# Kernel tuning notes

Measured on AMD Instinct MI355X. Metric: run time of the kernel, lower is better.

## Reference

```python
import jax, jax.numpy as jnp
import numpy as np

B, H, W, C = 16, 112, 112, 128
WS, SS, NH = 7, 3, 4  # window_size, shift_size, num_heads
EPS = 1e-5


def _ln(x, g, b):
    m = jnp.mean(x, axis=-1, keepdims=True)
    v = jnp.var(x, axis=-1, keepdims=True)
    return (x - m) * jax.lax.rsqrt(v + EPS) * g + b


def _rel_index(w):
    # standard Swin relative-position index, [w*w, w*w] int
    coords = np.stack(np.meshgrid(np.arange(w), np.arange(w), indexing='ij'))  # [2,w,w]
    flat = coords.reshape(2, -1)                      # [2, N]
    rel = (flat[:, :, None] - flat[:, None, :]).transpose(1, 2, 0)  # [N,N,2]
    rel = rel + (w - 1)
    return rel[..., 0] * (2 * w - 1) + rel[..., 1]


def _attn_mask(Hp, Wp, w, s):
    # standard Swin shifted-window attention mask, [nW, N, N] float32 (0 / -100)
    img = np.zeros((Hp, Wp))
    cnt = 0
    for hs in (slice(0, -w), slice(-w, -s), slice(-s, None)):
        for ws_ in (slice(0, -w), slice(-w, -s), slice(-s, None)):
            img[hs, ws_] = cnt
            cnt += 1
    mw = img.reshape(Hp // w, w, Wp // w, w).transpose(0, 2, 1, 3).reshape(-1, w * w)
    d = mw[:, None, :] - mw[:, :, None]
    return np.where(d != 0, -100.0, 0.0).astype(np.float32)


def setup_inputs() -> dict:
    key = jax.random.key(0)
    ks = jax.random.split(key, 8)
    f = lambda k, shape: jax.random.normal(k, shape, dtype=jnp.float32) * 0.02
    return dict(
        x=jax.random.normal(ks[0], (B, H, W, C), dtype=jnp.float32),
        norm1_g=jnp.ones((C,), jnp.float32), norm1_b=jnp.zeros((C,), jnp.float32),
        qkv_w=f(ks[1], (C, 3 * C)), qkv_b=jnp.zeros((3 * C,), jnp.float32),
        rel_table=f(ks[2], ((2 * WS - 1) ** 2, NH)),
        proj_w=f(ks[3], (C, C)), proj_b=jnp.zeros((C,), jnp.float32),
        norm2_g=jnp.ones((C,), jnp.float32), norm2_b=jnp.zeros((C,), jnp.float32),
        fc1_w=f(ks[4], (C, 4 * C)), fc1_b=jnp.zeros((4 * C,), jnp.float32),
        fc2_w=f(ks[5], (4 * C, C)), fc2_b=jnp.zeros((C,), jnp.float32),
    )


def reference(x, norm1_g, norm1_b, qkv_w, qkv_b, rel_table, proj_w, proj_b,
              norm2_g, norm2_b, fc1_w, fc1_b, fc2_w, fc2_b):
    w, s, nH = WS, SS, NH
    hd = C // nH
    N = w * w
    scale = hd ** -0.5

    shortcut = x
    xn = _ln(x, norm1_g, norm1_b)
    # cyclic shift (H, W already multiples of w -> no padding)
    xs = jnp.roll(xn, (-s, -s), axis=(1, 2)) if s > 0 else xn
    # window partition -> [B*nW, N, C]
    wins = xs.reshape(B, H // w, w, W // w, w, C).transpose(0, 1, 3, 2, 4, 5).reshape(-1, N, C)

    qkv = wins @ qkv_w + qkv_b  # [M, N, 3C]
    q, k, v = [t.reshape(-1, N, nH, hd).transpose(0, 2, 1, 3)
               for t in jnp.split(qkv, 3, axis=-1)]
    attn = jnp.einsum('mhqd,mhkd->mhqk', q * scale, k)  # [M, nH, N, N]

    idx = _rel_index(w)  # static numpy [N, N]
    bias = rel_table[idx.reshape(-1)].reshape(N, N, nH).transpose(2, 0, 1)  # [nH, N, N]
    attn = attn + bias[None]

    if s > 0:
        mask = jnp.asarray(_attn_mask(H, W, w, s))  # [nW, N, N] static
        nW = mask.shape[0]
        attn = (attn.reshape(B, nW, nH, N, N) + mask[None, :, None]).reshape(-1, nH, N, N)

    attn = jax.nn.softmax(attn, axis=-1)
    out = jnp.einsum('mhqk,mhkd->mhqd', attn, v).transpose(0, 2, 1, 3).reshape(-1, N, C)
    out = out @ proj_w + proj_b

    # window reverse + unshift
    x_attn = out.reshape(B, H // w, W // w, w, w, C).transpose(0, 1, 3, 2, 4, 5).reshape(B, H, W, C)
    if s > 0:
        x_attn = jnp.roll(x_attn, (s, s), axis=(1, 2))

    x1 = shortcut + x_attn
    xn2 = _ln(x1, norm2_g, norm2_b)
    hdd = jax.nn.gelu(xn2 @ fc1_w + fc1_b, approximate=False)  # torch nn.GELU (exact)
    return x1 + (hdd @ fc2_w + fc2_b)
```

## Files before the change

### kernel.cpp

```cpp
#include <hip/hip_runtime.h>
#include <stdint.h>

typedef unsigned short u16;
typedef unsigned int   u32;
typedef __attribute__((ext_vector_type(8))) short bh8;
typedef __attribute__((ext_vector_type(4))) float f32x4;

#define SCALE 0.17677669529663687f
#define MFMA  __builtin_amdgcn_mfma_f32_16x16x32_bf16

#define WS_QKV  0
#define WS_PROJ 49152
#define WS_F1   65536
#define WS_F2   131072
#define WS_M    196608
#define WS_QB   327680
#define WS_S1   328448
#define WS_T1   329472

__device__ __forceinline__ u16 f2bf(float f){
    u32 i; __builtin_memcpy(&i,&f,4); i += 0x7fffu + ((i>>16)&1u); return (u16)(i>>16);
}
__device__ __forceinline__ float bflo(u32 u){
    u32 i = u << 16; float f; __builtin_memcpy(&f,&i,4); return f;
}
__device__ __forceinline__ float bfhi(u32 u){
    u32 i = u & 0xffff0000u; float f; __builtin_memcpy(&f,&i,4); return f;
}
__device__ __forceinline__ u32 cvtpk(float lo, float hi){
    u32 r; asm("v_cvt_pk_bf16_f32 %0, %1, %2" : "=v"(r) : "v"(lo), "v"(hi)); return r;
}
__device__ __forceinline__ float rcpf(float v){
    float r; asm("v_rcp_f32 %0, %1" : "=v"(r) : "v"(v)); return r;
}
__device__ __forceinline__ float gelu_f(float x){
    float ax = fabsf(x);
    float z  = ax * 0.70710678118654752f;
    float t  = rcpf(fmaf(0.3275911f, z, 1.0f));
    float p  = t * fmaf(t, fmaf(t, fmaf(t, fmaf(t, 1.061405429f, -1.453152027f),
                                        1.421413741f), -0.284496736f), 0.254829592f);
    float e  = __expf(-z * z);
    float y  = fmaf(-p, e, 1.0f);
    return fmaf(0.5f * ax, y, 0.5f * x);
}
union BH8U { bh8 v; u32 u[4]; };

__global__ void prep_k(const float* __restrict__ qkvw, const float* __restrict__ projw,
                       const float* __restrict__ f1w,  const float* __restrict__ f2w,
                       const float* __restrict__ rel,  const float* __restrict__ qkvb,
                       const float* __restrict__ n2g,  const float* __restrict__ n2b,
                       const float* __restrict__ f1b,  u16* __restrict__ ws)
{
    int idx = blockIdx.x * 256 + threadIdx.x;
    if (idx < 49152) {
        int c = idx / 384, j = idx % 384;
        float v = qkvw[idx] * (j < 128 ? SCALE : 1.0f);
        ws[WS_QKV + j * 128 + c] = f2bf(v);
    } else if (idx < 65536) {
        int i = idx - 49152; int k = i >> 7, j = i & 127;
        int pk = (k & ~31) | ((k & 15) << 1) | ((k >> 4) & 1);
        ws[WS_PROJ + j * 128 + pk] = f2bf(projw[i]);
    } else if (idx < 131072) {
        int i = idx - 65536; int c = i >> 9, j = i & 511;
        ws[WS_F1 + j * 128 + c] = f2bf(f1w[i] * n2g[c]);
    } else if (idx < 196608) {
        int i = idx - 131072; int k = i >> 7, j = i & 127;
        int pk = (k & ~31) | ((k & 15) << 1) | ((k >> 4) & 1);
        ws[WS_F2 + j * 512 + pk] = f2bf(f2w[i]);
    } else if (idx < 262144) {
        int m = idx - 196608;
        int jr = m & 3, lane = (m >> 2) & 63, tct = (m >> 8) & 15;
        int h = (m >> 12) & 3, cls = (m >> 14) & 3;
        int rt = tct >> 2, ct = tct & 3;
        int row = rt * 16 + (lane >> 4) * 4 + jr, key = ct * 16 + (lane & 15);
        float v;
        if (row < 49 && key < 49) {
            int ri = row / 7, rc = row % 7, ki = key / 7, kc = key % 7;
            v = rel[((ri - ki + 6) * 13 + (rc - kc + 6)) * 4 + h];
            int rH = (cls & 2) ? (ri < 4 ? 1 : 2) : 0, rW = (cls & 1) ? (rc < 4 ? 1 : 2) : 0;
            int kH = (cls & 2) ? (ki < 4 ? 1 : 2) : 0, kW = (cls & 1) ? (kc < 4 ? 1 : 2) : 0;
            if (rH * 3 + rW != kH * 3 + kW) v -= 100.0f;
        } else v = -30000.0f;
        ((float*)(ws + WS_M))[m] = v;
    } else if (idx < 262528) {
        int j = idx - 262144;
        ((float*)(ws + WS_QB))[j] = qkvb[j] * (j < 128 ? SCALE : 1.0f);
    } else if (idx < 263040) {
        int j = idx - 262528;
        float s1 = 0.f, t1 = 0.f;
        for (int c = 0; c < 128; ++c) {
            float w = f1w[c * 512 + j];
            s1 = fmaf(n2g[c], w, s1);
            t1 = fmaf(n2b[c], w, t1);
        }
        ((float*)(ws + WS_S1))[j] = s1;
        ((float*)(ws + WS_T1))[j] = f1b[j] + t1;
    }
}

__global__ __launch_bounds__(256, 3) void swin_attn_k(
    const float* __restrict__ x, const float* __restrict__ n1g, const float* __restrict__ n1b,
    const float* __restrict__ projb, const u16* __restrict__ ws, float* __restrict__ out)
{
    __shared__ u16 arena[16384];
    __shared__ u16 vt[9216];
    const int tid = threadIdx.x, h = tid >> 6, lane = tid & 63;
    const int c15 = lane & 15, g = lane >> 4;
    const int m = blockIdx.x, b = m >> 8, hb = (m >> 4) & 15, wb = m & 15;
    const int cls = ((hb == 15) ? 2 : 0) | ((wb == 15) ? 1 : 0);
    const float* QB = (const float*)(ws + WS_QB);
    const float* Mb = (const float*)(ws + WS_M) + (size_t)((cls * 4 + h) * 16) * 256;

    {
        const int t = h * 16 + (lane >> 2), ss = lane & 3;
        if (t < 49) {
            const int td = (t * 37) >> 8, tm = t - td * 7;
            int hs = hb * 7 + td + 3;  if (hs >= 112) hs -= 112;
            int wsw = wb * 7 + tm + 3; if (wsw >= 112) wsw -= 112;
            const float* px = x + (size_t)((b * 112 + hs) * 112 + wsw) * 128 + ss * 32;
            float4 xv[8];
            #pragma unroll
            for (int i = 0; i < 8; ++i) xv[i] = *(const float4*)(px + i * 4);
            float s = 0.f, q = 0.f;
            #pragma unroll
            for (int i = 0; i < 8; ++i) {
                s += xv[i].x + xv[i].y + xv[i].z + xv[i].w;
                q += xv[i].x*xv[i].x + xv[i].y*xv[i].y + xv[i].z*xv[i].z + xv[i].w*xv[i].w;
            }
            s += __shfl_xor(s, 1); q += __shfl_xor(q, 1);
            s += __shfl_xor(s, 2); q += __shfl_xor(q, 2);
            float mean = s * (1.f/128.f), var = q * (1.f/128.f) - mean * mean;
            float rstd = rsqrtf(var + 1e-5f);
            const float* pg = n1g + ss * 32; const float* pb = n1b + ss * 32;
            #pragma unroll
            for (int i = 0; i < 4; ++i) {
                float4 a = xv[2*i], c = xv[2*i+1];
                float4 g1 = *(const float4*)(pg + i*8),  g2 = *(const float4*)(pg + i*8 + 4);
                float4 b1 = *(const float4*)(pb + i*8),  b2 = *(const float4*)(pb + i*8 + 4);
                uint4 w;
                w.x = cvtpk((a.x-mean)*rstd*g1.x + b1.x, (a.y-mean)*rstd*g1.y + b1.y);
                w.y = cvtpk((a.z-mean)*rstd*g1.z + b1.z, (a.w-mean)*rstd*g1.w + b1.w);
                w.z = cvtpk((c.x-mean)*rstd*g2.x + b2.x, (c.y-mean)*rstd*g2.y + b2.y);
                w.w = cvtpk((c.z-mean)*rstd*g2.z + b2.z, (c.w-mean)*rstd*g2.w + b2.w);
                *(uint4*)&arena[t * 136 + ss * 32 + i * 8] = w;
            }
        } else {
            #pragma unroll
            for (int i = 0; i < 4; ++i) *(uint4*)&arena[t * 136 + (lane & 3) * 32 + i * 8] = (uint4){0,0,0,0};
        }
    }
    __syncthreads();

    {
        bh8 avf[2][4];
        #pragma unroll
        for (int jt = 0; jt < 2; ++jt)
            #pragma unroll
            for (int kc = 0; kc < 4; ++kc)
                avf[jt][kc] = *(const bh8*)&ws[WS_QKV + (256 + h*32 + jt*16 + c15)*128 + kc*32 + g*8];
        const float vb0 = QB[256 + h*32 + c15], vb1 = QB[256 + h*32 + 16 + c15];
        #pragma unroll
        for (int tt = 0; tt < 4; ++tt) {
            bh8 xf[4];
            #pragma unroll
            for (int kc = 0; kc < 4; ++kc)
                xf[kc] = *(const bh8*)&arena[(tt*16 + c15)*136 + kc*32 + g*8];
            f32x4 D0 = {0,0,0,0}, D1 = {0,0,0,0};
            #pragma unroll
            for (int kc = 0; kc < 4; ++kc) { D0 = MFMA(xf[kc], avf[0][kc], D0, 0,0,0); D1 = MFMA(xf[kc], avf[1][kc], D1, 0,0,0); }
            uint2 p0, p1;
            p0.x = cvtpk(D0[0]+vb0, D0[1]+vb0); p0.y = cvtpk(D0[2]+vb0, D0[3]+vb0);
            p1.x = cvtpk(D1[0]+vb1, D1[1]+vb1); p1.y = cvtpk(D1[2]+vb1, D1[3]+vb1);
            *(uint2*)&vt[h*2304 + c15*72        + tt*16 + g*4] = p0;
            *(uint2*)&vt[h*2304 + (16+c15)*72   + tt*16 + g*4] = p1;
        }
    }

    bh8 qf[4], kf[4];
    {
        bh8 aqf[2][4], akf[2][4];
        #pragma unroll
        for (int jt = 0; jt < 2; ++jt)
            #pragma unroll
            for (int kc = 0; kc < 4; ++kc) {
                aqf[jt][kc] = *(const bh8*)&ws[WS_QKV + (      h*32 + jt*16 + c15)*128 + kc*32 + g*8];
                akf[jt][kc] = *(const bh8*)&ws[WS_QKV + (128 + h*32 + jt*16 + c15)*128 + kc*32 + g*8];
            }
        const float4 qb0 = *(const float4*)(QB + h*32 + g*4);
        const float4 qb1 = *(const float4*)(QB + h*32 + 16 + g*4);
        const float4 kb0 = *(const float4*)(QB + 128 + h*32 + g*4);
        const float4 kb1 = *(const float4*)(QB + 128 + h*32 + 16 + g*4);
        #pragma unroll
        for (int tt = 0; tt < 4; ++tt) {
            bh8 xf[4];
            #pragma unroll
            for (int kc = 0; kc < 4; ++kc)
                xf[kc] = *(const bh8*)&arena[(tt*16 + c15)*136 + kc*32 + g*8];
            f32x4 Dq0={0,0,0,0}, Dq1={0,0,0,0}, Dk0={0,0,0,0}, Dk1={0,0,0,0};
            #pragma unroll
            for (int kc = 0; kc < 4; ++kc) {
                Dq0 = MFMA(aqf[0][kc], xf[kc], Dq0, 0,0,0);
                Dq1 = MFMA(aqf[1][kc], xf[kc], Dq1, 0,0,0);
                Dk0 = MFMA(akf[0][kc], xf[kc], Dk0, 0,0,0);
                Dk1 = MFMA(akf[1][kc], xf[kc], Dk1, 0,0,0);
            }
            BH8U qu, ku;
            qu.u[0] = cvtpk(Dq0[0]+qb0.x, Dq0[1]+qb0.y); qu.u[1] = cvtpk(Dq0[2]+qb0.z, Dq0[3]+qb0.w);
            qu.u[2] = cvtpk(Dq1[0]+qb1.x, Dq1[1]+qb1.y); qu.u[3] = cvtpk(Dq1[2]+qb1.z, Dq1[3]+qb1.w);
            ku.u[0] = cvtpk(Dk0[0]+kb0.x, Dk0[1]+kb0.y); ku.u[1] = cvtpk(Dk0[2]+kb0.z, Dk0[3]+kb0.w);
            ku.u[2] = cvtpk(Dk1[0]+kb1.x, Dk1[1]+kb1.y); ku.u[3] = cvtpk(Dk1[2]+kb1.z, Dk1[3]+kb1.w);
            qf[tt] = qu.v; kf[tt] = ku.v;
        }
    }
    __syncthreads();

    f32x4 p[4][4]; f32x4 inv4[4];
    #pragma unroll
    for (int rt = 0; rt < 4; ++rt) {
        #pragma unroll
        for (int ct = 0; ct < 4; ++ct) {
            f32x4 macc = *(const f32x4*)(Mb + (rt*4 + ct)*256 + lane*4);
            p[rt][ct] = MFMA(qf[rt], kf[ct], macc, 0,0,0);
        }
        #pragma unroll
        for (int ct = 0; ct < 4; ++ct)
            #pragma unroll
            for (int jr = 0; jr < 4; ++jr) p[rt][ct][jr] = __expf(p[rt][ct][jr]);
        f32x4 t = p[rt][0] + p[rt][1] + p[rt][2] + p[rt][3];
        #pragma unroll
        for (int jr = 0; jr < 4; ++jr) {
            float v = t[jr];
            v += __shfl_xor(v, 1); v += __shfl_xor(v, 2);
            v += __shfl_xor(v, 4); v += __shfl_xor(v, 8);
            inv4[rt][jr] = rcpf(v + 1e-30f);
        }
    }

    char* Pbase = (char*)arena + h * 8192;
    #pragma unroll
    for (int rt = 0; rt < 4; ++rt)
        #pragma unroll
        for (int jr = 0; jr < 4; ++jr) {
            const int row = rt*16 + g*4 + jr, sw = (row & 7) << 4;
            #pragma unroll
            for (int ct = 0; ct < 4; ++ct)
                *(u16*)(Pbase + ((row*128 + (ct*16 + c15)*2) ^ sw)) = f2bf(p[rt][ct][jr]);
        }
    asm volatile("s_waitcnt lgkmcnt(0)" ::: "memory");

    f32x4 o[4][2];
    #pragma unroll
    for (int rt = 0; rt < 4; ++rt) { o[rt][0] = (f32x4){0,0,0,0}; o[rt][1] = (f32x4){0,0,0,0}; }
    {
        bh8 vf[2][2];
        #pragma unroll
        for (int ct = 0; ct < 2; ++ct)
            #pragma unroll
            for (int kc = 0; kc < 2; ++kc)
                vf[ct][kc] = *(const bh8*)&vt[h*2304 + (ct*16 + c15)*72 + kc*32 + g*8];
        #pragma unroll
        for (int rt = 0; rt < 4; ++rt) {
            const int row = rt*16 + c15, sw = (row & 7) << 4;
            #pragma unroll
            for (int kc = 0; kc < 2; ++kc) {
                bh8 pa = *(const bh8*)(Pbase + ((row*128 + kc*64 + g*16) ^ sw));
                o[rt][0] = MFMA(pa, vf[0][kc], o[rt][0], 0,0,0);
                o[rt][1] = MFMA(pa, vf[1][kc], o[rt][1], 0,0,0);
            }
        }
    }
    __syncthreads();

    #pragma unroll
    for (int rt = 0; rt < 4; ++rt)
        #pragma unroll
        for (int jr = 0; jr < 4; ++jr) {
            const int row = rt*16 + g*4 + jr;
            u32 pk_ = cvtpk(o[rt][0][jr] * inv4[rt][jr], o[rt][1][jr] * inv4[rt][jr]);
            *(u32*)&arena[row*136 + h*32 + 2*c15] = pk_;
        }
    __syncthreads();

    {
        bh8 wfp[2][4];
        #pragma unroll
        for (int ct2 = 0; ct2 < 2; ++ct2)
            #pragma unroll
            for (int kc = 0; kc < 4; ++kc)
                wfp[ct2][kc] = *(const bh8*)&ws[WS_PROJ + (h*32 + ct2*16 + c15)*128 + kc*32 + g*8];
        f32x4 pacc[4][2];
        #pragma unroll
        for (int rt = 0; rt < 4; ++rt) { pacc[rt][0] = (f32x4){0,0,0,0}; pacc[rt][1] = (f32x4){0,0,0,0}; }
        #pragma unroll
        for (int rt = 0; rt < 4; ++rt) {
            bh8 af[4];
            #pragma unroll
            for (int kc = 0; kc < 4; ++kc)
                af[kc] = *(const bh8*)&arena[(rt*16 + c15)*136 + kc*32 + g*8];
            #pragma unroll
            for (int kc = 0; kc < 4; ++kc) {
                pacc[rt][0] = MFMA(af[kc], wfp[0][kc], pacc[rt][0], 0,0,0);
                pacc[rt][1] = MFMA(af[kc], wfp[1][kc], pacc[rt][1], 0,0,0);
            }
        }
        const int col0 = h*32 + c15, col1 = col0 + 16;
        const float pb0 = projb[col0], pb1 = projb[col1];
        #pragma unroll
        for (int rt = 0; rt < 4; ++rt)
            #pragma unroll
            for (int jr = 0; jr < 4; ++jr) {
                const int t = rt*16 + g*4 + jr;
                if (t < 49) {
                    const int td = (t * 37) >> 8, tm = t - td * 7;
                    int hs = hb*7 + td + 3;  if (hs >= 112) hs -= 112;
                    int wsw = wb*7 + tm + 3; if (wsw >= 112) wsw -= 112;
                    const size_t base = (size_t)((b*112 + hs)*112 + wsw) * 128;
                    out[base + col0] = pacc[rt][0][jr] + pb0 + x[base + col0];
                    out[base + col1] = pacc[rt][1][jr] + pb1 + x[base + col1];
                }
            }
    }
}

__global__ __launch_bounds__(256, 4) void swin_mlp_k(
    float* __restrict__ xio, const float* __restrict__ f2b, const u16* __restrict__ ws)
{
    __shared__ u16 xnb[64 * 136];
    __shared__ u16 hbuf[64 * 136];
    __shared__ float2 stats[64];
    const int tid = threadIdx.x, w = tid >> 6, lane = tid & 63;
    const int c15 = lane & 15, g = lane >> 4;
    const size_t tok0 = (size_t)blockIdx.x * 64;
    const float* S1 = (const float*)(ws + WS_S1);
    const float* T1 = (const float*)(ws + WS_T1);

    {
        const int t = w * 16 + (lane >> 2), ss = lane & 3;
        const float* px = xio + (tok0 + t) * 128 + ss * 32;
        float4 xv[8];
        #pragma unroll
        for (int i = 0; i < 8; ++i) xv[i] = *(const float4*)(px + i * 4);
        float s = 0.f, q = 0.f;
        #pragma unroll
        for (int i = 0; i < 8; ++i) {
            s += xv[i].x + xv[i].y + xv[i].z + xv[i].w;
            q += xv[i].x*xv[i].x + xv[i].y*xv[i].y + xv[i].z*xv[i].z + xv[i].w*xv[i].w;
        }
        s += __shfl_xor(s, 1); q += __shfl_xor(q, 1);
        s += __shfl_xor(s, 2); q += __shfl_xor(q, 2);
        float mean = s * (1.f/128.f), var = q * (1.f/128.f) - mean * mean;
        float rstd = rsqrtf(var + 1e-5f);
        #pragma unroll
        for (int i = 0; i < 4; ++i) {
            float4 a = xv[2*i], c = xv[2*i+1];
            uint4 wv;
            wv.x = cvtpk(a.x, a.y); wv.y = cvtpk(a.z, a.w);
            wv.z = cvtpk(c.x, c.y); wv.w = cvtpk(c.z, c.w);
            *(uint4*)&xnb[t * 136 + ss * 32 + i * 8] = wv;
        }
        if (ss == 0) stats[t] = (float2){rstd, rstd * mean};
    }
    __syncthreads();

    f32x4 acc[4][2];
    #pragma unroll
    for (int rt = 0; rt < 4; ++rt) { acc[rt][0] = (f32x4){0,0,0,0}; acc[rt][1] = (f32x4){0,0,0,0}; }

    #pragma unroll
    for (int chunk = 0; chunk < 4; ++chunk) {
        bh8 wf1[2][4];
        #pragma unroll
        for (int jt = 0; jt < 2; ++jt)
            #pragma unroll
            for (int kc = 0; kc < 4; ++kc)
                wf1[jt][kc] = *(const bh8*)&ws[WS_F1 + (chunk*128 + w*32 + jt*16 + c15)*128 + kc*32 + g*8];
        const int j0 = chunk*128 + w*32 + c15;
        const float s1a = S1[j0], s1b = S1[j0 + 16];
        const float t1a = T1[j0], t1b = T1[j0 + 16];
        if (chunk) __syncthreads();
        #pragma unroll
        for (int rt = 0; rt < 4; ++rt) {
            bh8 af[4];
            #pragma unroll
            for (int kc = 0; kc < 4; ++kc)
                af[kc] = *(const bh8*)&xnb[(rt*16 + c15)*136 + kc*32 + g*8];
            f32x4 D0 = {0,0,0,0}, D1 = {0,0,0,0};
            #pragma unroll
            for (int kc = 0; kc < 4; ++kc) { D0 = MFMA(af[kc], wf1[0][kc], D0, 0,0,0); D1 = MFMA(af[kc], wf1[1][kc], D1, 0,0,0); }
            #pragma unroll
            for (int jr = 0; jr < 4; ++jr) {
                const int row = rt*16 + g*4 + jr;
                float2 st = stats[row];
                float h0 = gelu_f(fmaf(st.x, D0[jr], fmaf(-st.y, s1a, t1a)));
                float h1 = gelu_f(fmaf(st.x, D1[jr], fmaf(-st.y, s1b, t1b)));
                *(u32*)&hbuf[row*136 + w*32 + 2*c15] = cvtpk(h0, h1);
            }
        }
        __syncthreads();
        bh8 wf2[2][4];
        #pragma unroll
        for (int ct2 = 0; ct2 < 2; ++ct2)
            #pragma unroll
            for (int kc = 0; kc < 4; ++kc)
                wf2[ct2][kc] = *(const bh8*)&ws[WS_F2 + (w*32 + ct2*16 + c15)*512 + chunk*128 + kc*32 + g*8];
        #pragma unroll
        for (int rt = 0; rt < 4; ++rt) {
            bh8 ha[4];
            #pragma unroll
            for (int kc = 0; kc < 4; ++kc)
                ha[kc] = *(const bh8*)&hbuf[(rt*16 + c15)*136 + kc*32 + g*8];
            #pragma unroll
            for (int kc = 0; kc < 4; ++kc) {
                acc[rt][0] = MFMA(ha[kc], wf2[0][kc], acc[rt][0], 0,0,0);
                acc[rt][1] = MFMA(ha[kc], wf2[1][kc], acc[rt][1], 0,0,0);
            }
        }
    }

    const int col0 = w*32 + c15, col1 = col0 + 16;
    const float cb0 = f2b[col0], cb1 = f2b[col1];
    #pragma unroll
    for (int rt = 0; rt < 4; ++rt)
        #pragma unroll
        for (int jr = 0; jr < 4; ++jr) {
            const size_t r = (tok0 + rt*16 + g*4 + jr) * 128;
            xio[r + col0] += acc[rt][0][jr] + cb0;
            xio[r + col1] += acc[rt][1][jr] + cb1;
        }
}

extern "C" void kernel_launch(void* const* d_in, const int* in_sizes, int n_in,
                              void* d_out, int out_size, void* d_ws, size_t ws_size,
                              hipStream_t stream)
{
    const float* x    = (const float*)d_in[0];
    const float* n1g  = (const float*)d_in[1];
    const float* n1b  = (const float*)d_in[2];
    const float* qkvw = (const float*)d_in[3];
    const float* qkvb = (const float*)d_in[4];
    const float* rel  = (const float*)d_in[5];
    const float* pw   = (const float*)d_in[6];
    const float* pb   = (const float*)d_in[7];
    const float* n2g  = (const float*)d_in[8];
    const float* n2b  = (const float*)d_in[9];
    const float* f1w  = (const float*)d_in[10];
    const float* f1b  = (const float*)d_in[11];
    const float* f2w  = (const float*)d_in[12];
    const float* f2b  = (const float*)d_in[13];
    float* out = (float*)d_out;
    u16* ws = (u16*)d_ws;

    prep_k<<<1028, 256, 0, stream>>>(qkvw, pw, f1w, f2w, rel, qkvb, n2g, n2b, f1b, ws);
    swin_attn_k<<<4096, 256, 0, stream>>>(x, n1g, n1b, pb, ws, out);
    swin_mlp_k<<<3136, 256, 0, stream>>>(out, f2b, ws);
}
```

Baseline: 274.5 us.

## Retile MLP kernel to 128-token blocks with 8 waves and prefetched fc1 weights

The MLP kernel now handles 128 tokens per 512-thread block, with each wave owning 16 hidden/output columns instead of 32. Each weight fragment loaded from global memory is therefore reused across twice as many token rows, which halves weight traffic per token. The next chunk's fc1 weights are prefetched into registers while the current chunk runs, and the fc2 weight packing permutation is dropped to match the new layout. In exchange, hidden activations are stored as scalar 16-bit LDS writes instead of packed pairs, LDS use doubles per block, and occupancy is capped at two 512-thread blocks per CU.

```diff
diff --git a/kernel.cpp b/kernel.cpp
--- a/kernel.cpp
+++ b/kernel.cpp
@@ -20,12 +20,6 @@
 
 __device__ __forceinline__ u16 f2bf(float f){
     u32 i; __builtin_memcpy(&i,&f,4); i += 0x7fffu + ((i>>16)&1u); return (u16)(i>>16);
-}
-__device__ __forceinline__ float bflo(u32 u){
-    u32 i = u << 16; float f; __builtin_memcpy(&f,&i,4); return f;
-}
-__device__ __forceinline__ float bfhi(u32 u){
-    u32 i = u & 0xffff0000u; float f; __builtin_memcpy(&f,&i,4); return f;
 }
 __device__ __forceinline__ u32 cvtpk(float lo, float hi){
     u32 r; asm("v_cvt_pk_bf16_f32 %0, %1, %2" : "=v"(r) : "v"(lo), "v"(hi)); return r;
@@ -65,8 +59,7 @@
         ws[WS_F1 + j * 128 + c] = f2bf(f1w[i] * n2g[c]);
     } else if (idx < 196608) {
         int i = idx - 131072; int k = i >> 7, j = i & 127;
-        int pk = (k & ~31) | ((k & 15) << 1) | ((k >> 4) & 1);
-        ws[WS_F2 + j * 512 + pk] = f2bf(f2w[i]);
+        ws[WS_F2 + j * 512 + k] = f2bf(f2w[i]);
     } else if (idx < 262144) {
         int m = idx - 196608;
         int jr = m & 3, lane = (m >> 2) & 63, tct = (m >> 8) & 15;
@@ -322,20 +315,20 @@
     }
 }
 
-__global__ __launch_bounds__(256, 4) void swin_mlp_k(
+__global__ __launch_bounds__(512, 2) void swin_mlp_k(
     float* __restrict__ xio, const float* __restrict__ f2b, const u16* __restrict__ ws)
 {
-    __shared__ u16 xnb[64 * 136];
-    __shared__ u16 hbuf[64 * 136];
-    __shared__ float2 stats[64];
+    __shared__ u16 xnb[128 * 136];
+    __shared__ u16 hbuf[128 * 136];
+    __shared__ float2 stats[128];
     const int tid = threadIdx.x, w = tid >> 6, lane = tid & 63;
     const int c15 = lane & 15, g = lane >> 4;
-    const size_t tok0 = (size_t)blockIdx.x * 64;
+    const size_t tok0 = (size_t)blockIdx.x * 128;
     const float* S1 = (const float*)(ws + WS_S1);
     const float* T1 = (const float*)(ws + WS_T1);
 
     {
-        const int t = w * 16 + (lane >> 2), ss = lane & 3;
+        const int t = tid >> 2, ss = tid & 3;
         const float* px = xio + (tok0 + t) * 128 + ss * 32;
         float4 xv[8];
         #pragma unroll
@@ -362,70 +355,72 @@
     }
     __syncthreads();
 
-    f32x4 acc[4][2];
-    #pragma unroll
-    for (int rt = 0; rt < 4; ++rt) { acc[rt][0] = (f32x4){0,0,0,0}; acc[rt][1] = (f32x4){0,0,0,0}; }
+    const int jc = w * 16 + c15;
+    f32x4 acc[8];
+    #pragma unroll
+    for (int rt = 0; rt < 8; ++rt) acc[rt] = (f32x4){0,0,0,0};
+
+    bh8 wf1a[4];
+    #pragma unroll
+    for (int kc = 0; kc < 4; ++kc)
+        wf1a[kc] = *(const bh8*)&ws[WS_F1 + jc*128 + kc*32 + g*8];
 
     #pragma unroll
     for (int chunk = 0; chunk < 4; ++chunk) {
-        bh8 wf1[2][4];
-        #pragma unroll
-        for (int jt = 0; jt < 2; ++jt)
-            #pragma unroll
-            for (int kc = 0; kc < 4; ++kc)
-                wf1[jt][kc] = *(const bh8*)&ws[WS_F1 + (chunk*128 + w*32 + jt*16 + c15)*128 + kc*32 + g*8];
-        const int j0 = chunk*128 + w*32 + c15;
-        const float s1a = S1[j0], s1b = S1[j0 + 16];
-        const float t1a = T1[j0], t1b = T1[j0 + 16];
-        if (chunk) __syncthreads();
-        #pragma unroll
-        for (int rt = 0; rt < 4; ++rt) {
+        bh8 wf2[4], wf1n[4];
+        #pragma unroll
+        for (int kc = 0; kc < 4; ++kc)
+            wf2[kc] = *(const bh8*)&ws[WS_F2 + jc*512 + chunk*128 + kc*32 + g*8];
+        if (chunk < 3) {
+            #pragma unroll
+            for (int kc = 0; kc < 4; ++kc)
+                wf1n[kc] = *(const bh8*)&ws[WS_F1 + ((chunk+1)*128 + jc)*128 + kc*32 + g*8];
+        }
+        const float s1 = S1[chunk*128 + jc], t1 = T1[chunk*128 + jc];
+
+        #pragma unroll
+        for (int rt = 0; rt < 8; ++rt) {
             bh8 af[4];
             #pragma unroll
             for (int kc = 0; kc < 4; ++kc)
                 af[kc] = *(const bh8*)&xnb[(rt*16 + c15)*136 + kc*32 + g*8];
-            f32x4 D0 = {0,0,0,0}, D1 = {0,0,0,0};
-            #pragma unroll
-            for (int kc = 0; kc < 4; ++kc) { D0 = MFMA(af[kc], wf1[0][kc], D0, 0,0,0); D1 = MFMA(af[kc], wf1[1][kc], D1, 0,0,0); }
+            f32x4 D = {0,0,0,0};
+            #pragma unroll
+            for (int kc = 0; kc < 4; ++kc) D = MFMA(af[kc], wf1a[kc], D, 0,0,0);
             #pragma unroll
             for (int jr = 0; jr < 4; ++jr) {
                 const int row = rt*16 + g*4 + jr;
                 float2 st = stats[row];
-                float h0 = gelu_f(fmaf(st.x, D0[jr], fmaf(-st.y, s1a, t1a)));
-                float h1 = gelu_f(fmaf(st.x, D1[jr], fmaf(-st.y, s1b, t1b)));
-                *(u32*)&hbuf[row*136 + w*32 + 2*c15] = cvtpk(h0, h1);
+                float hv = gelu_f(fmaf(st.x, D[jr], fmaf(-st.y, s1, t1)));
+                hbuf[row*136 + jc] = f2bf(hv);
             }
         }
         __syncthreads();
-        bh8 wf2[2][4];
-        #pragma unroll
-        for (int ct2 = 0; ct2 < 2; ++ct2)
-            #pragma unroll
-            for (int kc = 0; kc < 4; ++kc)
-                wf2[ct2][kc] = *(const bh8*)&ws[WS_F2 + (w*32 + ct2*16 + c15)*512 + chunk*128 + kc*32 + g*8];
-        #pragma unroll
-        for (int rt = 0; rt < 4; ++rt) {
+
+        #pragma unroll
+        for (int rt = 0; rt < 8; ++rt) {
             bh8 ha[4];
             #pragma unroll
             for (int kc = 0; kc < 4; ++kc)
                 ha[kc] = *(const bh8*)&hbuf[(rt*16 + c15)*136 + kc*32 + g*8];
             #pragma unroll
-            for (int kc = 0; kc < 4; ++kc) {
-                acc[rt][0] = MFMA(ha[kc], wf2[0][kc], acc[rt][0], 0,0,0);
-                acc[rt][1] = MFMA(ha[kc], wf2[1][kc], acc[rt][1], 0,0,0);
-            }
-        }
-    }
-
-    const int col0 = w*32 + c15, col1 = col0 + 16;
-    const float cb0 = f2b[col0], cb1 = f2b[col1];
-    #pragma unroll
-    for (int rt = 0; rt < 4; ++rt)
+            for (int kc = 0; kc < 4; ++kc)
+                acc[rt] = MFMA(ha[kc], wf2[kc], acc[rt], 0,0,0);
+        }
+        if (chunk < 3) {
+            __syncthreads();
+            #pragma unroll
+            for (int kc = 0; kc < 4; ++kc) wf1a[kc] = wf1n[kc];
+        }
+    }
+
+    const float cb = f2b[jc];
+    #pragma unroll
+    for (int rt = 0; rt < 8; ++rt)
         #pragma unroll
         for (int jr = 0; jr < 4; ++jr) {
             const size_t r = (tok0 + rt*16 + g*4 + jr) * 128;
-            xio[r + col0] += acc[rt][0][jr] + cb0;
-            xio[r + col1] += acc[rt][1][jr] + cb1;
+            xio[r + jc] += acc[rt][jr] + cb;
         }
 }
 
@@ -452,5 +447,5 @@
 
     prep_k<<<1028, 256, 0, stream>>>(qkvw, pw, f1w, f2w, rel, qkvb, n2g, n2b, f1b, ws);
     swin_attn_k<<<4096, 256, 0, stream>>>(x, n1g, n1b, pb, ws, out);
-    swin_mlp_k<<<3136, 256, 0, stream>>>(out, f2b, ws);
-}
+    swin_mlp_k<<<1568, 512, 0, stream>>>(out, f2b, ws);
+}
```

After: 284.9 us. +3.8%, slower.

## Double-buffer MLP hidden tile and software-pipeline fc1/fc2 with prefetched weights

Applied to the files above, without the earlier changes.

The MLP kernel now ping-pongs between two shared hidden buffers. FC1 of the next chunk is interleaved with FC2 of the previous one, which cuts the barriers per chunk from two to one. Weight fragments for fc1 are prefetched one chunk ahead, and the first ones load before the LayerNorm stats pass. This adds a second 17KB LDS buffer and lowers launch bounds from 4 to 3 blocks per CU, trading occupancy for overlap of MFMA, GELU and global loads.

```diff
diff --git a/kernel.cpp b/kernel.cpp
--- a/kernel.cpp
+++ b/kernel.cpp
@@ -20,12 +20,6 @@
 
 __device__ __forceinline__ u16 f2bf(float f){
     u32 i; __builtin_memcpy(&i,&f,4); i += 0x7fffu + ((i>>16)&1u); return (u16)(i>>16);
-}
-__device__ __forceinline__ float bflo(u32 u){
-    u32 i = u << 16; float f; __builtin_memcpy(&f,&i,4); return f;
-}
-__device__ __forceinline__ float bfhi(u32 u){
-    u32 i = u & 0xffff0000u; float f; __builtin_memcpy(&f,&i,4); return f;
 }
 __device__ __forceinline__ u32 cvtpk(float lo, float hi){
     u32 r; asm("v_cvt_pk_bf16_f32 %0, %1, %2" : "=v"(r) : "v"(lo), "v"(hi)); return r;
@@ -322,11 +316,12 @@
     }
 }
 
-__global__ __launch_bounds__(256, 4) void swin_mlp_k(
+__global__ __launch_bounds__(256, 3) void swin_mlp_k(
     float* __restrict__ xio, const float* __restrict__ f2b, const u16* __restrict__ ws)
 {
     __shared__ u16 xnb[64 * 136];
-    __shared__ u16 hbuf[64 * 136];
+    __shared__ u16 hb0[64 * 136];
+    __shared__ u16 hb1[64 * 136];
     __shared__ float2 stats[64];
     const int tid = threadIdx.x, w = tid >> 6, lane = tid & 63;
     const int c15 = lane & 15, g = lane >> 4;
@@ -334,8 +329,15 @@
     const float* S1 = (const float*)(ws + WS_S1);
     const float* T1 = (const float*)(ws + WS_T1);
 
-    {
-        const int t = w * 16 + (lane >> 2), ss = lane & 3;
+    bh8 wf1[2][4];
+    #pragma unroll
+    for (int jt = 0; jt < 2; ++jt)
+        #pragma unroll
+        for (int kc = 0; kc < 4; ++kc)
+            wf1[jt][kc] = *(const bh8*)&ws[WS_F1 + (w*32 + jt*16 + c15)*128 + kc*32 + g*8];
+
+    {
+        const int t = tid >> 2, ss = tid & 3;
         const float* px = xio + (tok0 + t) * 128 + ss * 32;
         float4 xv[8];
         #pragma unroll
@@ -365,19 +367,25 @@
     f32x4 acc[4][2];
     #pragma unroll
     for (int rt = 0; rt < 4; ++rt) { acc[rt][0] = (f32x4){0,0,0,0}; acc[rt][1] = (f32x4){0,0,0,0}; }
-
-    #pragma unroll
-    for (int chunk = 0; chunk < 4; ++chunk) {
-        bh8 wf1[2][4];
+    bh8 wf2[2][4];
+
+    auto LD_W1 = [&](int chunk) {
         #pragma unroll
         for (int jt = 0; jt < 2; ++jt)
             #pragma unroll
             for (int kc = 0; kc < 4; ++kc)
                 wf1[jt][kc] = *(const bh8*)&ws[WS_F1 + (chunk*128 + w*32 + jt*16 + c15)*128 + kc*32 + g*8];
-        const int j0 = chunk*128 + w*32 + c15;
-        const float s1a = S1[j0], s1b = S1[j0 + 16];
-        const float t1a = T1[j0], t1b = T1[j0 + 16];
-        if (chunk) __syncthreads();
+    };
+    auto LD_W2 = [&](int chunk) {
+        #pragma unroll
+        for (int ct2 = 0; ct2 < 2; ++ct2)
+            #pragma unroll
+            for (int kc = 0; kc < 4; ++kc)
+                wf2[ct2][kc] = *(const bh8*)&ws[WS_F2 + (w*32 + ct2*16 + c15)*512 + chunk*128 + kc*32 + g*8];
+    };
+    auto FC1 = [&](int chunk, u16* hb) {
+        const float s1a = S1[chunk*128 + w*32 + c15], s1b = S1[chunk*128 + w*32 + 16 + c15];
+        const float t1a = T1[chunk*128 + w*32 + c15], t1b = T1[chunk*128 + w*32 + 16 + c15];
         #pragma unroll
         for (int rt = 0; rt < 4; ++rt) {
             bh8 af[4];
@@ -393,29 +401,44 @@
                 float2 st = stats[row];
                 float h0 = gelu_f(fmaf(st.x, D0[jr], fmaf(-st.y, s1a, t1a)));
                 float h1 = gelu_f(fmaf(st.x, D1[jr], fmaf(-st.y, s1b, t1b)));
-                *(u32*)&hbuf[row*136 + w*32 + 2*c15] = cvtpk(h0, h1);
-            }
-        }
-        __syncthreads();
-        bh8 wf2[2][4];
-        #pragma unroll
-        for (int ct2 = 0; ct2 < 2; ++ct2)
-            #pragma unroll
-            for (int kc = 0; kc < 4; ++kc)
-                wf2[ct2][kc] = *(const bh8*)&ws[WS_F2 + (w*32 + ct2*16 + c15)*512 + chunk*128 + kc*32 + g*8];
+                *(u32*)&hb[row*136 + w*32 + 2*c15] = cvtpk(h0, h1);
+            }
+        }
+    };
+    auto FC2 = [&](const u16* hb) {
         #pragma unroll
         for (int rt = 0; rt < 4; ++rt) {
             bh8 ha[4];
             #pragma unroll
             for (int kc = 0; kc < 4; ++kc)
-                ha[kc] = *(const bh8*)&hbuf[(rt*16 + c15)*136 + kc*32 + g*8];
+                ha[kc] = *(const bh8*)&hb[(rt*16 + c15)*136 + kc*32 + g*8];
             #pragma unroll
             for (int kc = 0; kc < 4; ++kc) {
                 acc[rt][0] = MFMA(ha[kc], wf2[0][kc], acc[rt][0], 0,0,0);
                 acc[rt][1] = MFMA(ha[kc], wf2[1][kc], acc[rt][1], 0,0,0);
             }
         }
-    }
+    };
+
+    FC1(0, hb0);
+    LD_W1(1);
+    __syncthreads();
+    LD_W2(0);
+    FC1(1, hb1);
+    LD_W1(2);
+    FC2(hb0);
+    __syncthreads();
+    LD_W2(1);
+    FC1(2, hb0);
+    LD_W1(3);
+    FC2(hb1);
+    __syncthreads();
+    LD_W2(2);
+    FC1(3, hb1);
+    FC2(hb0);
+    __syncthreads();
+    LD_W2(3);
+    FC2(hb1);
 
     const int col0 = w*32 + c15, col1 = col0 + 16;
     const float cb0 = f2b[col0], cb1 = f2b[col1];
```

Result: faster. 252.6 us, median of 2 (-8.0%).
